# Kernel tuning notes

Measured on AMD Instinct MI355X. Metric: run time of the kernel, lower is better.

Reference implementation:

```python
import jax, jax.numpy as jnp
import numpy as np

B, S, D, H = 2, 2048, 1024, 16
E = D // H  # per-head dim_q = dim_k = 64
LN_EPS = 1e-5


def setup_inputs() -> dict:
    key = jax.random.key(0)
    ks = jax.random.split(key, 12)
    s_in = 1.0 / np.sqrt(D)
    s_cat = 1.0 / np.sqrt(H * E)
    return {
        "q": jax.random.normal(ks[0], (B, S, D), jnp.float32),
        "k": jax.random.normal(ks[1], (B, S, D), jnp.float32),
        "v": jax.random.normal(ks[2], (B, S, D), jnp.float32),
        # stacked per-head projection weights [H, D, E] (acts as x @ W + b per head)
        "Wq": jax.random.uniform(ks[3], (H, D, E), jnp.float32, -s_in, s_in),
        "bq": jax.random.uniform(ks[4], (H, E), jnp.float32, -s_in, s_in),
        "Wk": jax.random.uniform(ks[5], (H, D, E), jnp.float32, -s_in, s_in),
        "bk": jax.random.uniform(ks[6], (H, E), jnp.float32, -s_in, s_in),
        "Wv": jax.random.uniform(ks[7], (H, D, E), jnp.float32, -s_in, s_in),
        "bv": jax.random.uniform(ks[8], (H, E), jnp.float32, -s_in, s_in),
        # output linear: [H*E, D]
        "Wo": jax.random.uniform(ks[9], (H * E, D), jnp.float32, -s_cat, s_cat),
        "bo": jax.random.uniform(ks[10], (D,), jnp.float32, -s_cat, s_cat),
        # LayerNorm affine params
        "gamma": jnp.ones((D,), jnp.float32),
        "beta": jnp.zeros((D,), jnp.float32),
    }


def _attention(q, k, v, Wq, bq, Wk, bk, Wv, bv, Wo, bo, gamma, beta):
    # per-head projections: [B,H,S,E]
    qh = jnp.einsum('bsd,hde->bhse', q, Wq) + bq[None, :, None, :]
    kh = jnp.einsum('bsd,hde->bhse', k, Wk) + bk[None, :, None, :]
    vh = jnp.einsum('bsd,hde->bhse', v, Wv) + bv[None, :, None, :]
    scale = jnp.asarray(E, qh.dtype) ** 0.5
    scores = jnp.einsum('bhse,bhte->bhst', qh, kh) / scale  # [B,H,S,S]
    attn = jax.nn.softmax(scores, axis=-1)
    ctx = jnp.einsum('bhst,bhte->bhse', attn, vh)  # [B,H,S,E]
    # concat heads -> [B,S,H*E], then output linear
    cat = ctx.transpose(0, 2, 1, 3).reshape(q.shape[0], q.shape[1], H * E)
    out = cat @ Wo + bo  # [B,S,D]
    # Residual (dropout = identity in eval) + LayerNorm
    x = q + out
    mu = jnp.mean(x, axis=-1, keepdims=True)
    var = jnp.mean((x - mu) ** 2, axis=-1, keepdims=True)
    return (x - mu) * jax.lax.rsqrt(var + LN_EPS) * gamma + beta


def reference(q, k, v, Wq, bq, Wk, bk, Wv, bv, Wo, bo, gamma, beta):
    return _attention(q, k, v, Wq, bq, Wk, bk, Wv, bv, Wo, bo, gamma, beta)
```

## Files before the change

kernel.cpp:

```cpp
#include <hip/hip_runtime.h>
#include <stdint.h>

#define B_  2
#define S_  2048
#define D_  1024
#define H_  16
#define E_  64
#define BH_ 32
#define M_  4096
#define NSPLIT 4
#define KCHUNK (S_ / NSPLIT)

typedef __bf16 bf16x8 __attribute__((ext_vector_type(8)));
typedef float  f32x4  __attribute__((ext_vector_type(4)));
typedef float  f32x16 __attribute__((ext_vector_type(16)));
typedef unsigned short u16;

#define QSCALE 0.180336880f

#define EXP2(x) __builtin_amdgcn_exp2f(x)

__device__ __forceinline__ u16 f2bf(float f) {
  uint32_t u = __builtin_bit_cast(uint32_t, f);
  u = (u + 0x7FFFu + ((u >> 16) & 1u)) >> 16;
  return (u16)u;
}

__device__ __forceinline__ uint32_t pkbf(float lo, float hi) {
  __bf16 a = (__bf16)lo, b = (__bf16)hi;
  return (uint32_t)__builtin_bit_cast(u16, a) |
         ((uint32_t)__builtin_bit_cast(u16, b) << 16);
}

__device__ __forceinline__ bf16x8 load_frag(const u16* p) {
  uint4 v = *(const uint4*)p;
  return __builtin_bit_cast(bf16x8, v);
}

__device__ __forceinline__ float bf2f(u16 u) {
  return __builtin_bit_cast(float, (uint32_t)u << 16);
}

__device__ __forceinline__ void gload16(const void* g, void* l) {
  auto gp = reinterpret_cast<const uint32_t __attribute__((address_space(1)))*>(
      reinterpret_cast<uintptr_t>(g));
  auto lp = reinterpret_cast<uint32_t __attribute__((address_space(3)))*>(
      reinterpret_cast<uintptr_t>(l));
  __builtin_amdgcn_global_load_lds(gp, lp, 16, 0, 0);
}

__global__ __launch_bounds__(256) void transpose_cvt3w(
    const float* __restrict__ Wq, const float* __restrict__ Wk,
    const float* __restrict__ Wv, u16* __restrict__ out)
{
  __shared__ float tile[32][33];
  const int z = blockIdx.z, sel = z >> 4, b = z & 15;
  const float* in = (sel == 0 ? Wq : (sel == 1 ? Wk : Wv)) + (size_t)b * 65536;
  u16* o = out + (size_t)sel * 1048576 + (size_t)b * 65536;
  const int R = 1024, C = 64;
  const int c0 = blockIdx.x * 32, r0 = blockIdx.y * 32;
  const int tx = threadIdx.x, ty = threadIdx.y;
#pragma unroll
  for (int j = 0; j < 32; j += 8)
    tile[ty + j][tx] = in[(size_t)(r0 + ty + j) * C + c0 + tx];
  __syncthreads();
#pragma unroll
  for (int j = 0; j < 32; j += 8)
    o[(size_t)(c0 + ty + j) * R + r0 + tx] = f2bf(tile[tx][ty + j]);
}

__global__ __launch_bounds__(256) void transpose_cvt(
    const float* __restrict__ in, u16* __restrict__ out, int R, int C)
{
  __shared__ float tile[32][33];
  const int c0 = blockIdx.x * 32, r0 = blockIdx.y * 32;
  const int tx = threadIdx.x, ty = threadIdx.y;
#pragma unroll
  for (int j = 0; j < 32; j += 8)
    tile[ty + j][tx] = in[(size_t)(r0 + ty + j) * C + c0 + tx];
  __syncthreads();
#pragma unroll
  for (int j = 0; j < 32; j += 8)
    out[(size_t)(c0 + ty + j) * R + r0 + tx] = f2bf(tile[tx][ty + j]);
}

template<int MODE>
__global__ __launch_bounds__(256) void gemm128(
    const float* __restrict__ Aq, const float* __restrict__ Ak,
    const float* __restrict__ Av, const u16* __restrict__ Abf,
    const u16* __restrict__ Bt,
    const float* __restrict__ b0, const float* __restrict__ b1,
    const float* __restrict__ b2, const float* __restrict__ resid,
    u16* __restrict__ outQ, u16* __restrict__ outK, u16* __restrict__ outV,
    float* __restrict__ outX)
{
  __shared__ __align__(16) u16 As[128 * 64];
  __shared__ __align__(16) u16 Bs[128 * 64];
  const int K  = D_;
  const int id = blockIdx.x;
  const int xcd = id & 7, slot = id >> 3;
  int mi_, ni_;
  if (MODE == 0) { ni_ = slot % 24; mi_ = (xcd << 2) | (slot / 24); }
  else           { ni_ = slot & 7;  mi_ = (xcd << 2) | (slot >> 3); }
  const int m0 = mi_ * 128;
  const int n0 = ni_ * 128;
  const int tid = threadIdx.x;
  const int w = tid >> 6, l = tid & 63;
  const int wr = w >> 1, wc = w & 1;
  const int ql = l & 31, h2 = l >> 5;

  const u16* Buse = Bt;
  const float* bias = b0;
  const float* Af = nullptr;
  const u16* Ause = Abf;
  int third = 0, nloc = n0;
  if (MODE == 0) {
    third = n0 >> 10;
    nloc  = n0 & 1023;
    Af    = third == 0 ? Aq : (third == 1 ? Ak : Av);
    Buse  = Bt + (size_t)third * D_ * D_;
    bias  = third == 0 ? b0 : (third == 1 ? b1 : b2);
  }

  const int rr = l >> 3, gce = ((l & 7) ^ (l >> 3)) * 8;
  const float* aptrf[4];
  const u16*   aptr[4];
  const u16*   bptr[4];
#pragma unroll
  for (int c = 0; c < 4; ++c) {
    const int chunk = w * 4 + c;
    if (MODE == 0)
      aptrf[c] = Af + (size_t)(m0 + chunk * 8 + rr) * K + gce;
    else
      aptr[c]  = Ause + (size_t)(m0 + chunk * 8 + rr) * K + gce;
    bptr[c] = Buse + (size_t)(nloc + chunk * 8 + rr) * K + gce;
  }

  const int swz = ql & 7;
  f32x16 acc[2][2] = {};

  float4 a0[4], a1[4];
  if (MODE == 0) {
#pragma unroll
    for (int c = 0; c < 4; ++c) {
      a0[c] = *(const float4*)(aptrf[c]);
      a1[c] = *(const float4*)(aptrf[c] + 4);
    }
  }

  for (int k0 = 0; k0 < K; k0 += 64) {
    __syncthreads();
#pragma unroll
    for (int c = 0; c < 4; ++c) {
      const int chunk = w * 4 + c;
      if (MODE == 0) {
        uint4 pw;
        pw.x = pkbf(a0[c].x, a0[c].y);
        pw.y = pkbf(a0[c].z, a0[c].w);
        pw.z = pkbf(a1[c].x, a1[c].y);
        pw.w = pkbf(a1[c].z, a1[c].w);
        *(uint4*)(&As[chunk * 8 * 64 + l * 8]) = pw;
      } else {
        gload16(aptr[c] + k0, &As[chunk * 8 * 64]);
      }
      gload16(bptr[c] + k0, &Bs[chunk * 8 * 64]);
    }
    if (MODE == 0 && k0 + 64 < K) {
#pragma unroll
      for (int c = 0; c < 4; ++c) {
        a0[c] = *(const float4*)(aptrf[c] + k0 + 64);
        a1[c] = *(const float4*)(aptrf[c] + k0 + 68);
      }
    }
    __syncthreads();
#pragma unroll
    for (int ks = 0; ks < 4; ++ks) {
      const int ch = ((ks * 2 + h2) ^ swz) * 8;
      bf16x8 af[2], bf[2];
#pragma unroll
      for (int mi = 0; mi < 2; ++mi)
        af[mi] = load_frag(&As[(wr * 64 + mi * 32 + ql) * 64 + ch]);
#pragma unroll
      for (int ni = 0; ni < 2; ++ni)
        bf[ni] = load_frag(&Bs[(wc * 64 + ni * 32 + ql) * 64 + ch]);
#pragma unroll
      for (int mi = 0; mi < 2; ++mi)
#pragma unroll
        for (int ni = 0; ni < 2; ++ni)
          acc[mi][ni] = __builtin_amdgcn_mfma_f32_32x32x16_bf16(
              af[mi], bf[ni], acc[mi][ni], 0, 0, 0);
    }
  }

  const int rbase = m0 + wr * 64;
  const int cbase = nloc + wc * 64;
#pragma unroll
  for (int mi = 0; mi < 2; ++mi) {
#pragma unroll
    for (int ni = 0; ni < 2; ++ni) {
      const int col = cbase + ni * 32 + ql;
      const float bv = bias[col];
      if (MODE == 0) {
        const int h = col >> 6, e = col & 63;
        if (third < 2) {
          u16* dst = third == 0 ? outQ : outK;
          const float sc = third == 0 ? QSCALE : 1.f;
#pragma unroll
          for (int r = 0; r < 16; ++r) {
            int row = rbase + mi * 32 + (r & 3) + 8 * (r >> 2) + 4 * h2;
            int bb = row >> 11, s = row & (S_ - 1);
            dst[((size_t)(bb * H_ + h) * S_ + s) * E_ + e] =
                f2bf((acc[mi][ni][r] + bv) * sc);
          }
        } else {
#pragma unroll
          for (int g = 0; g < 4; ++g) {
            int s0 = rbase + mi * 32 + ((g >> 1) << 4) + (h2 << 3) + ((g & 1) << 2);
            int bb = s0 >> 11, srel = s0 & (S_ - 1);
            ushort4 o;
            o.x = f2bf(acc[mi][ni][4 * g + 0] + bv);
            o.y = f2bf(acc[mi][ni][4 * g + 1] + bv);
            o.z = f2bf(acc[mi][ni][4 * g + 2] + bv);
            o.w = f2bf(acc[mi][ni][4 * g + 3] + bv);
            *(ushort4*)(&outV[((size_t)(bb * H_ + h) * E_ + e) * S_ + srel]) = o;
          }
        }
      } else {
#pragma unroll
        for (int r = 0; r < 16; ++r) {
          int row = rbase + mi * 32 + (r & 3) + 8 * (r >> 2) + 4 * h2;
          size_t idx = (size_t)row * D_ + col;
          outX[idx] = acc[mi][ni][r] + bv + resid[idx];
        }
      }
    }
  }
}

__global__ __launch_bounds__(256, 4) void attn_kernel(
    const u16* __restrict__ qh, const u16* __restrict__ kh,
    const u16* __restrict__ vT, u16* __restrict__ pA, u16* __restrict__ pB,
    float* __restrict__ ml)
{
  __shared__ __align__(16) u16 Ks[2][64 * 64];
  __shared__ __align__(16) u16 Vs[2][64 * 64];
  const int o = blockIdx.x;
  const int xcd = o & 7, slot = o >> 3;
  const int bh    = (xcd << 2) | (slot >> 6);
  const int rem   = slot & 63;
  const int split = rem >> 4;
  const int q0    = (rem & 15) * 128;
  const int kst = split * KCHUNK;
  const int tid = threadIdx.x;
  const int w = tid >> 6, l = tid & 63;
  const int ql = l & 31;
  const int h  = l >> 5;
  const int qg = q0 + w * 32 + ql;

  const size_t PSZ = (size_t)BH_ * S_ * E_;
  u16* po = split < 2 ? pA + (size_t)split * PSZ : pB + (size_t)(split - 2) * PSZ;

  const u16* qrow = qh + ((size_t)bh * S_ + qg) * E_;
  bf16x8 bq_[4];
#pragma unroll
  for (int es = 0; es < 4; ++es)
    bq_[es] = load_frag(qrow + es * 16 + h * 8);

  f32x16 oacc[2] = {};
  float lloc = 0.f;

  const int srow = w * 8 + (l >> 3);
  const int gch  = (l & 7) ^ (l >> 3);
  const u16* kbase = kh + (size_t)bh * S_ * E_;
  const u16* vbase = vT + (size_t)bh * E_ * S_;
  const int swz = (ql & 7);

  auto stage = [&](int buf, int t0) {
#pragma unroll
    for (int p = 0; p < 2; ++p) {
      gload16(kbase + (size_t)(t0 + p * 32 + srow) * E_ + gch * 8,
              &Ks[buf][p * 2048 + w * 512]);
      gload16(vbase + (size_t)(p * 32 + srow) * S_ + t0 + gch * 8,
              &Vs[buf][p * 2048 + w * 512]);
    }
  };

  stage(0, kst);
  int cur = 0;
  for (int t0 = kst; t0 < kst + KCHUNK; t0 += 64) {
    __syncthreads();
    if (t0 + 64 < kst + KCHUNK) stage(cur ^ 1, t0 + 64);

#pragma unroll
    for (int kt = 0; kt < 2; ++kt) {
      f32x16 sacc = {};
#pragma unroll
      for (int es = 0; es < 4; ++es) {
        bf16x8 ak = load_frag(
            &Ks[cur][(kt * 32 + ql) * 64 + (((es * 2 + h) ^ swz) * 8)]);
        sacc = __builtin_amdgcn_mfma_f32_32x32x16_bf16(ak, bq_[es], sacc, 0, 0, 0);
      }

      float ps0 = 0.f, ps1 = 0.f, ps2 = 0.f, ps3 = 0.f;
#pragma unroll
      for (int i = 0; i < 16; i += 4) {
        float p0 = EXP2(sacc[i + 0]); sacc[i + 0] = p0; ps0 += p0;
        float p1 = EXP2(sacc[i + 1]); sacc[i + 1] = p1; ps1 += p1;
        float p2 = EXP2(sacc[i + 2]); sacc[i + 2] = p2; ps2 += p2;
        float p3 = EXP2(sacc[i + 3]); sacc[i + 3] = p3; ps3 += p3;
      }
      lloc += (ps0 + ps1) + (ps2 + ps3);

#pragma unroll
      for (int c2 = 0; c2 < 2; ++c2) {
        uint4 pw;
        pw.x = pkbf(sacc[8 * c2 + 0], sacc[8 * c2 + 1]);
        pw.y = pkbf(sacc[8 * c2 + 2], sacc[8 * c2 + 3]);
        pw.z = pkbf(sacc[8 * c2 + 4], sacc[8 * c2 + 5]);
        pw.w = pkbf(sacc[8 * c2 + 6], sacc[8 * c2 + 7]);
        bf16x8 pb = __builtin_bit_cast(bf16x8, pw);
        const int vch = ((kt * 2 + c2) * 2 + h) ^ swz;
#pragma unroll
        for (int eb = 0; eb < 2; ++eb) {
          bf16x8 av = load_frag(&Vs[cur][(eb * 32 + ql) * 64 + vch * 8]);
          oacc[eb] = __builtin_amdgcn_mfma_f32_32x32x16_bf16(av, pb, oacc[eb], 0, 0, 0);
        }
      }
    }
    cur ^= 1;
  }

  float l_ = lloc + __shfl_xor(lloc, 32);
  const float inv = 1.f / l_;
  const size_t rowbase = ((size_t)bh * S_ + qg) * E_;
#pragma unroll
  for (int eb = 0; eb < 2; ++eb)
#pragma unroll
    for (int g = 0; g < 4; ++g) {
      ushort4 o2;
      o2.x = f2bf(oacc[eb][4 * g + 0] * inv);
      o2.y = f2bf(oacc[eb][4 * g + 1] * inv);
      o2.z = f2bf(oacc[eb][4 * g + 2] * inv);
      o2.w = f2bf(oacc[eb][4 * g + 3] * inv);
      *(ushort4*)(&po[rowbase + eb * 32 + g * 8 + h * 4]) = o2;
    }
  if (h == 0)
    ml[(size_t)(split * BH_ + bh) * S_ + qg] = l_;
}

__global__ __launch_bounds__(256) void combine_kernel(
    const u16* __restrict__ pA, const u16* __restrict__ pB,
    const float* __restrict__ ml, u16* __restrict__ cat)
{
  const int idx = blockIdx.x * 256 + threadIdx.x;
  const int e  = (idx & 15) * 4;
  const int s  = (idx >> 4) & (S_ - 1);
  const int bh = idx >> 15;
  const size_t row = (size_t)bh * S_ + s;
  const size_t PSZ = (size_t)BH_ * S_ * E_;

  float li[NSPLIT], W = 0.f;
#pragma unroll
  for (int i = 0; i < NSPLIT; ++i) {
    li[i] = ml[(size_t)(i * BH_ + bh) * S_ + s];
    W += li[i];
  }
  const float invW = 1.f / W;

  float acc0 = 0.f, acc1 = 0.f, acc2 = 0.f, acc3 = 0.f;
#pragma unroll
  for (int i = 0; i < NSPLIT; ++i) {
    const u16* p = i < 2 ? pA + (size_t)i * PSZ : pB + (size_t)(i - 2) * PSZ;
    ushort4 u = *(const ushort4*)(&p[row * E_ + e]);
    const float wi = li[i] * invW;
    acc0 += wi * bf2f(u.x);
    acc1 += wi * bf2f(u.y);
    acc2 += wi * bf2f(u.z);
    acc3 += wi * bf2f(u.w);
  }
  ushort4 o;
  o.x = f2bf(acc0); o.y = f2bf(acc1); o.z = f2bf(acc2); o.w = f2bf(acc3);
  *(ushort4*)(&cat[((size_t)(bh >> 4) * S_ + s) * D_ + (bh & 15) * E_ + e]) = o;
}

__global__ __launch_bounds__(256) void layernorm_kernel(
    float* __restrict__ x, const float* __restrict__ gamma,
    const float* __restrict__ beta)
{
  __shared__ float red[8];
  const int row = blockIdx.x;
  float* p = x + (size_t)row * D_;
  const int tid = threadIdx.x;
  float4 v = *(const float4*)(p + tid * 4);
  float s  = v.x + v.y + v.z + v.w;
  float sq = v.x * v.x + v.y * v.y + v.z * v.z + v.w * v.w;
#pragma unroll
  for (int d = 1; d < 64; d <<= 1) {
    s  += __shfl_xor(s, d);
    sq += __shfl_xor(sq, d);
  }
  const int w = tid >> 6, l = tid & 63;
  if (l == 0) { red[w] = s; red[4 + w] = sq; }
  __syncthreads();
  float S1 = red[0] + red[1] + red[2] + red[3];
  float S2 = red[4] + red[5] + red[6] + red[7];
  float mu  = S1 * (1.f / D_);
  float var = S2 * (1.f / D_) - mu * mu;
  float rinv = rsqrtf(var + 1e-5f);
  float4 g  = *(const float4*)(gamma + tid * 4);
  float4 bt = *(const float4*)(beta + tid * 4);
  float4 o;
  o.x = (v.x - mu) * rinv * g.x + bt.x;
  o.y = (v.y - mu) * rinv * g.y + bt.y;
  o.z = (v.z - mu) * rinv * g.z + bt.z;
  o.w = (v.w - mu) * rinv * g.w + bt.w;
  *(float4*)(p + tid * 4) = o;
}

extern "C" void kernel_launch(void* const* d_in, const int* in_sizes, int n_in,
                              void* d_out, int out_size, void* d_ws, size_t ws_size,
                              hipStream_t stream) {
  (void)in_sizes; (void)n_in; (void)out_size; (void)ws_size;
  const float* q     = (const float*)d_in[0];
  const float* k     = (const float*)d_in[1];
  const float* v     = (const float*)d_in[2];
  const float* Wq    = (const float*)d_in[3];
  const float* bq    = (const float*)d_in[4];
  const float* Wk    = (const float*)d_in[5];
  const float* bk    = (const float*)d_in[6];
  const float* Wv    = (const float*)d_in[7];
  const float* bv    = (const float*)d_in[8];
  const float* Wo    = (const float*)d_in[9];
  const float* bo    = (const float*)d_in[10];
  const float* gamma = (const float*)d_in[11];
  const float* beta  = (const float*)d_in[12];

  char* ws = (char*)d_ws;
  u16* cat    = (u16*)ws;
  u16* Wt     = (u16*)(ws + 25165824);
  u16* WoT    = (u16*)(ws + 31457280);
  u16* qhb    = (u16*)(ws + 33554432);
  u16* khb    = (u16*)(ws + 41943040);
  u16* vTb    = (u16*)(ws + 50331648);
  u16*   pA  = (u16*)d_out;
  u16*   pB  = (u16*)(ws + 8388608);
  float* mlb = (float*)(ws + 25165824);
  float* x   = (float*)d_out;

  dim3 tb(32, 8);
  transpose_cvt3w<<<dim3(2, 32, 48), tb, 0, stream>>>(Wq, Wk, Wv, Wt);
  transpose_cvt<<<dim3(32, 32, 1), tb, 0, stream>>>(Wo, WoT, 1024, 1024);

  gemm128<0><<<768, 256, 0, stream>>>(q, k, v, nullptr, Wt, bq, bk, bv, nullptr,
                                      qhb, khb, vTb, nullptr);
  attn_kernel<<<2048, 256, 0, stream>>>(qhb, khb, vTb, pA, pB, mlb);
  combine_kernel<<<4096, 256, 0, stream>>>(pA, pB, mlb, cat);
  gemm128<1><<<256, 256, 0, stream>>>(nullptr, nullptr, nullptr, cat, WoT, bo,
                                      nullptr, nullptr, q,
                                      nullptr, nullptr, nullptr, x);
  layernorm_kernel<<<4096, 256, 0, stream>>>(x, gamma, beta);
}
```

Before: 150.8 us.

## Double-buffer LDS tiles in projection GEMM to overlap loads with MFMA

The projection/output GEMM now uses two LDS buffers for the A and B tiles. While MFMAs consume the current buffer, the next K-slice is written into the other one, and one of the two barriers per iteration is removed. This is meant to hide global-to-LDS latency behind compute. In exchange it doubles LDS use (64KB per block), which may reduce occupancy. The direct global-to-LDS loads (gload16) also need correct waitcnt handling before the single barrier.

```diff
diff --git a/kernel.cpp b/kernel.cpp
--- a/kernel.cpp
+++ b/kernel.cpp
@@ -94,8 +94,8 @@
     u16* __restrict__ outQ, u16* __restrict__ outK, u16* __restrict__ outV,
     float* __restrict__ outX)
 {
-  __shared__ __align__(16) u16 As[128 * 64];
-  __shared__ __align__(16) u16 Bs[128 * 64];
+  __shared__ __align__(16) u16 As[2][128 * 64];
+  __shared__ __align__(16) u16 Bs[2][128 * 64];
   const int K  = D_;
   const int id = blockIdx.x;
   const int xcd = id & 7, slot = id >> 3;
@@ -138,51 +138,77 @@
 
   const int swz = ql & 7;
   f32x16 acc[2][2] = {};
-
   float4 a0[4], a1[4];
+
   if (MODE == 0) {
 #pragma unroll
     for (int c = 0; c < 4; ++c) {
       a0[c] = *(const float4*)(aptrf[c]);
       a1[c] = *(const float4*)(aptrf[c] + 4);
     }
-  }
-
+#pragma unroll
+    for (int c = 0; c < 4; ++c) {
+      const int chunk = w * 4 + c;
+      uint4 pw;
+      pw.x = pkbf(a0[c].x, a0[c].y);
+      pw.y = pkbf(a0[c].z, a0[c].w);
+      pw.z = pkbf(a1[c].x, a1[c].y);
+      pw.w = pkbf(a1[c].z, a1[c].w);
+      *(uint4*)(&As[0][chunk * 8 * 64 + l * 8]) = pw;
+    }
+  }
+#pragma unroll
+  for (int c = 0; c < 4; ++c) {
+    const int chunk = w * 4 + c;
+    if (MODE == 1) gload16(aptr[c], &As[0][chunk * 8 * 64]);
+    gload16(bptr[c], &Bs[0][chunk * 8 * 64]);
+  }
+  if (MODE == 0) {
+#pragma unroll
+    for (int c = 0; c < 4; ++c) {
+      a0[c] = *(const float4*)(aptrf[c] + 64);
+      a1[c] = *(const float4*)(aptrf[c] + 68);
+    }
+  }
+
+  int cur = 0;
   for (int k0 = 0; k0 < K; k0 += 64) {
     __syncthreads();
-#pragma unroll
-    for (int c = 0; c < 4; ++c) {
-      const int chunk = w * 4 + c;
-      if (MODE == 0) {
-        uint4 pw;
-        pw.x = pkbf(a0[c].x, a0[c].y);
-        pw.y = pkbf(a0[c].z, a0[c].w);
-        pw.z = pkbf(a1[c].x, a1[c].y);
-        pw.w = pkbf(a1[c].z, a1[c].w);
-        *(uint4*)(&As[chunk * 8 * 64 + l * 8]) = pw;
-      } else {
-        gload16(aptr[c] + k0, &As[chunk * 8 * 64]);
-      }
-      gload16(bptr[c] + k0, &Bs[chunk * 8 * 64]);
-    }
-    if (MODE == 0 && k0 + 64 < K) {
+    const int nxt = k0 + 64;
+    if (nxt < K) {
 #pragma unroll
       for (int c = 0; c < 4; ++c) {
-        a0[c] = *(const float4*)(aptrf[c] + k0 + 64);
-        a1[c] = *(const float4*)(aptrf[c] + k0 + 68);
-      }
-    }
-    __syncthreads();
+        const int chunk = w * 4 + c;
+        if (MODE == 0) {
+          uint4 pw;
+          pw.x = pkbf(a0[c].x, a0[c].y);
+          pw.y = pkbf(a0[c].z, a0[c].w);
+          pw.z = pkbf(a1[c].x, a1[c].y);
+          pw.w = pkbf(a1[c].z, a1[c].w);
+          *(uint4*)(&As[cur ^ 1][chunk * 8 * 64 + l * 8]) = pw;
+        } else {
+          gload16(aptr[c] + nxt, &As[cur ^ 1][chunk * 8 * 64]);
+        }
+        gload16(bptr[c] + nxt, &Bs[cur ^ 1][chunk * 8 * 64]);
+      }
+      if (MODE == 0 && nxt + 64 < K) {
+#pragma unroll
+        for (int c = 0; c < 4; ++c) {
+          a0[c] = *(const float4*)(aptrf[c] + nxt + 64);
+          a1[c] = *(const float4*)(aptrf[c] + nxt + 68);
+        }
+      }
+    }
 #pragma unroll
     for (int ks = 0; ks < 4; ++ks) {
       const int ch = ((ks * 2 + h2) ^ swz) * 8;
       bf16x8 af[2], bf[2];
 #pragma unroll
       for (int mi = 0; mi < 2; ++mi)
-        af[mi] = load_frag(&As[(wr * 64 + mi * 32 + ql) * 64 + ch]);
+        af[mi] = load_frag(&As[cur][(wr * 64 + mi * 32 + ql) * 64 + ch]);
 #pragma unroll
       for (int ni = 0; ni < 2; ++ni)
-        bf[ni] = load_frag(&Bs[(wc * 64 + ni * 32 + ql) * 64 + ch]);
+        bf[ni] = load_frag(&Bs[cur][(wc * 64 + ni * 32 + ql) * 64 + ch]);
 #pragma unroll
       for (int mi = 0; mi < 2; ++mi)
 #pragma unroll
@@ -190,6 +216,7 @@
           acc[mi][ni] = __builtin_amdgcn_mfma_f32_32x32x16_bf16(
               af[mi], bf[ni], acc[mi][ni], 0, 0, 0);
     }
+    cur ^= 1;
   }
 
   const int rbase = m0 + wr * 64;
```

Measured after the change: 155.7 us. 3.2% more time.
